# Optimization experiments

Hardware: AMD Instinct MI355X
Metric: run time of the kernel (lower is better)

Reference implementation:

```python
import jax, jax.numpy as jnp
import numpy as np

K, D, H, PD = 512, 512, 512, 128  # nodes, input_dim(=hidden), hidden_dim, pair_dim
P = K * (K - 1)
EPS = 1e-5


def setup_inputs() -> dict:
    key = jax.random.key(0)
    ks = jax.random.split(key, 16)
    s = lambda n: 1.0 / np.sqrt(n)
    return {
        "x": jax.random.normal(ks[0], (K, D), jnp.float32),
        "pair_feats": jax.random.normal(ks[1], (P, PD), jnp.float32),
        "W_att": jax.random.normal(ks[2], (1, 2 * D + PD), jnp.float32) * s(2 * D + PD),
        "b_att": jnp.zeros((1,), jnp.float32),
        "W_obj": jax.random.normal(ks[3], (H, D), jnp.float32) * s(D),
        "b_obj": jnp.zeros((H,), jnp.float32),
        "W_pair": jax.random.normal(ks[4], (H, PD), jnp.float32) * s(PD),
        "b_pair": jnp.zeros((H,), jnp.float32),
        "ln_g": jnp.ones((H,), jnp.float32),
        "ln_b": jnp.zeros((H,), jnp.float32),
        "W1": jax.random.normal(ks[5], (H, H), jnp.float32) * s(H),
        "b1": jnp.zeros((H,), jnp.float32),
        "W2": jax.random.normal(ks[6], (H, H), jnp.float32) * s(H),
        "b2": jnp.zeros((H,), jnp.float32),
    }


def _layernorm(v, g, b):
    mu = jnp.mean(v, axis=-1, keepdims=True)
    var = jnp.mean(jnp.square(v - mu), axis=-1, keepdims=True)
    return g * (v - mu) * jax.lax.rsqrt(var + EPS) + b


def reference(x, pair_feats, W_att, b_att, W_obj, b_obj, W_pair, b_pair,
              ln_g, ln_b, W1, b1, W2, b2):
    k = x.shape[0]
    # j index for each (i, slot t): j = t + (t >= i), i.e. all j != i, ascending
    t = jnp.arange(k - 1)
    j_idx = t[None, :] + (t[None, :] >= jnp.arange(k)[:, None])  # [K, K-1]

    # split the att_mlp weight to avoid materializing cat([x_i, x_j, pair])
    wa, wb, wc = W_att[0, :D], W_att[0, D:2 * D], W_att[0, 2 * D:]
    sa = x @ wa                                           # [K]
    sb = x @ wb                                           # [K]
    pf = pair_feats.reshape(k, k - 1, PD)                 # row-major (i, j!=i)
    sc = jnp.einsum('ktp,p->kt', pf, wc)                  # [K, K-1]
    alpha = jax.nn.sigmoid(sa[:, None] + sb[j_idx] + sc + b_att[0])  # [K, K-1]

    oj = x @ W_obj.T + b_obj                              # [K, H]
    pp = jnp.einsum('ktp,hp->kth', pf, W_pair) + b_pair   # [K, K-1, H]
    messages = jnp.mean(alpha[..., None] * (oj[j_idx] + pp), axis=1)  # [K, H]

    out = _layernorm(x + messages, ln_g, ln_b)
    ffn = jax.nn.relu(out @ W1.T + b1) @ W2.T + b2
    out = _layernorm(out + ffn, ln_g, ln_b)
    return out
```

## Files before the change

### kernel.cpp

```cpp
#include <hip/hip_runtime.h>
#include <math.h>

#define KK 512
#define DD 512
#define HH 512
#define PD 128
#define KM1 511
#define LN_EPS 1e-5f
#define NCHUNK 4
#define CHUNK_T 128

typedef __attribute__((ext_vector_type(8))) short sh8;
typedef __attribute__((ext_vector_type(4))) short sh4;
typedef __attribute__((ext_vector_type(4))) float fx4;

#define MFMA16(a, b, c) __builtin_amdgcn_mfma_f32_16x16x32_bf16(a, b, c, 0, 0, 0)

__device__ __forceinline__ float wave_reduce_sum(float v) {
    #pragma unroll
    for (int off = 32; off > 0; off >>= 1)
        v += __shfl_xor(v, off, 64);
    return v;
}

__device__ __forceinline__ float half_reduce_sum(float v) {
    #pragma unroll
    for (int off = 16; off > 0; off >>= 1)
        v += __shfl_xor(v, off, 64);
    return v;
}

__device__ __forceinline__ short f2bf(float f) {
    unsigned u = __float_as_uint(f);
    u += 0x7fff + ((u >> 16) & 1);
    return (short)(u >> 16);
}

__device__ __forceinline__ sh8 load_cvt8(const float* p) {
    float4 v0 = *(const float4*)p;
    float4 v1 = *(const float4*)(p + 4);
    sh8 r;
    r[0] = f2bf(v0.x); r[1] = f2bf(v0.y); r[2] = f2bf(v0.z); r[3] = f2bf(v0.w);
    r[4] = f2bf(v1.x); r[5] = f2bf(v1.y); r[6] = f2bf(v1.z); r[7] = f2bf(v1.w);
    return r;
}

__global__ __launch_bounds__(256) void prep_w(const float* __restrict__ W_obj,
                                              const float* __restrict__ W_pair,
                                              const float* __restrict__ W1,
                                              const float* __restrict__ W2,
                                              short* __restrict__ W_objb,
                                              short* __restrict__ W_pairb,
                                              short* __restrict__ W1b,
                                              short* __restrict__ W2b) {
    int i = blockIdx.x * 256 + threadIdx.x;
    const float* src; short* dst; int j;
    if (i < 65536)       { src = W_obj;  dst = W_objb;  j = i; }
    else if (i < 81920)  { src = W_pair; dst = W_pairb; j = i - 65536; }
    else if (i < 147456) { src = W1;     dst = W1b;     j = i - 81920; }
    else                 { src = W2;     dst = W2b;     j = i - 147456; }
    float4 v = ((const float4*)src)[j];
    sh4 s;
    s[0] = f2bf(v.x); s[1] = f2bf(v.y); s[2] = f2bf(v.z); s[3] = f2bf(v.w);
    ((sh4*)dst)[j] = s;
}

__global__ __launch_bounds__(64) void sab_kernel(const float* __restrict__ x,
                                                 const float* __restrict__ W_att,
                                                 float* __restrict__ sa,
                                                 float* __restrict__ sb) {
    int k = blockIdx.x;
    int lane = threadIdx.x;
    const float4* xr = (const float4*)(x + (size_t)k * DD);
    const float4* wa = (const float4*)(W_att);
    const float4* wb = (const float4*)(W_att + DD);
    float pa = 0.f, pb = 0.f;
    #pragma unroll
    for (int i = 0; i < 2; i++) {
        float4 xv = xr[lane + i * 64];
        float4 av = wa[lane + i * 64];
        float4 bv = wb[lane + i * 64];
        pa += xv.x * av.x + xv.y * av.y + xv.z * av.z + xv.w * av.w;
        pb += xv.x * bv.x + xv.y * bv.y + xv.z * bv.z + xv.w * bv.w;
    }
    pa = wave_reduce_sum(pa);
    pb = wave_reduce_sum(pb);
    if (lane == 0) { sa[k] = pa; sb[k] = pb; }
}

__global__ __launch_bounds__(512) void pair_pass_kernel(
    const float* __restrict__ pf, const float* __restrict__ sa,
    const float* __restrict__ sb, const float* __restrict__ W_att,
    const float* __restrict__ b_att, float* __restrict__ A,
    float* __restrict__ apf_part, float* __restrict__ asum_part) {
    int k = blockIdx.x;
    int chunk = blockIdx.y;
    int tbase = chunk * CHUNK_T;
    int tid = threadIdx.x;
    int w = tid >> 6, lane = tid & 63;
    int h = lane >> 5, c = lane & 31;
    int g = w * 2 + h;

    float4 wc4 = ((const float4*)(W_att + 2 * DD))[c];
    float sak = sa[k];
    float batt = b_att[0];
    const float4* pfk = (const float4*)(pf + (size_t)k * KM1 * PD);

    float4 v[8];
    int tr[8];
    #pragma unroll
    for (int it = 0; it < 8; it++) {
        int t = tbase + it * 16 + g;
        tr[it] = t;
        int tc = t < KM1 ? t : KM1 - 1;
        v[it] = pfk[(size_t)tc * 32 + c];
    }

    float a0 = 0.f, a1 = 0.f, a2 = 0.f, a3 = 0.f, asl = 0.f;
    #pragma unroll
    for (int it = 0; it < 8; it++) {
        float part = v[it].x * wc4.x + v[it].y * wc4.y + v[it].z * wc4.z + v[it].w * wc4.w;
        part = half_reduce_sum(part);
        int t = tr[it];
        int j = t + (t >= k);
        int jj = j < KK ? j : KK - 1;
        float z = sak + sb[jj] + part + batt;
        float alpha = (t < KM1) ? 1.f / (1.f + __expf(-z)) : 0.f;
        if (c == 0 && t < KM1) A[(size_t)k * KK + j] = alpha;
        a0 += alpha * v[it].x;
        a1 += alpha * v[it].y;
        a2 += alpha * v[it].z;
        a3 += alpha * v[it].w;
        asl += alpha;
    }

    __shared__ float apf_s[16][128];
    __shared__ float asum_s[16];
    apf_s[g][4 * c + 0] = a0;
    apf_s[g][4 * c + 1] = a1;
    apf_s[g][4 * c + 2] = a2;
    apf_s[g][4 * c + 3] = a3;
    if (c == 0) asum_s[g] = asl;
    __syncthreads();
    if (tid < PD) {
        float s = 0.f;
        #pragma unroll
        for (int i = 0; i < 16; i++) s += apf_s[i][tid];
        apf_part[((size_t)chunk * KK + k) * PD + tid] = s;
    }
    if (tid == 0) {
        float s = 0.f;
        #pragma unroll
        for (int i = 0; i < 16; i++) s += asum_s[i];
        asum_part[(size_t)chunk * KK + k] = s;
        if (chunk == 0) A[(size_t)k * KK + k] = 0.f;
    }
}

__global__ __launch_bounds__(128) void k_oj(const float* __restrict__ x,
                                            const short* __restrict__ W_objb,
                                            const float* __restrict__ b_obj,
                                            short* __restrict__ ojT) {
    int m0 = blockIdx.y * 32, n0 = blockIdx.x * 32;
    int tid = threadIdx.x;
    int wv = tid >> 6, l = tid & 63;
    int lr = l & 15, lk = (l >> 4) * 8;
    int mw = m0 + wv * 16;
    fx4 acc[2] = {};
    for (int k0 = 0; k0 < DD; k0 += 32) {
        sh8 a  = load_cvt8(&x[(size_t)(mw + lr) * DD + k0 + lk]);
        sh8 b0 = *(const sh8*)&W_objb[(size_t)(n0 + lr) * DD + k0 + lk];
        sh8 b1 = *(const sh8*)&W_objb[(size_t)(n0 + 16 + lr) * DD + k0 + lk];
        acc[0] = MFMA16(a, b0, acc[0]);
        acc[1] = MFMA16(a, b1, acc[1]);
    }
    __shared__ short tile[32][40];
    int lm4 = (l >> 4) * 4;
    #pragma unroll
    for (int cf = 0; cf < 2; cf++) {
        int col = cf * 16 + lr;
        float bo = b_obj[n0 + col];
        #pragma unroll
        for (int r = 0; r < 4; r++)
            tile[col][wv * 16 + lm4 + r] = f2bf(acc[cf][r] + bo);
    }
    __syncthreads();
    int col = tid >> 2, ro = (tid & 3) * 8;
    *(sh8*)&ojT[(size_t)(n0 + col) * KK + m0 + ro] = *(sh8*)&tile[col][ro];
}

__global__ __launch_bounds__(128) void k_msg(const float* __restrict__ A,
                                             const short* __restrict__ ojT,
                                             const float* __restrict__ apf_part,
                                             const short* __restrict__ W_pairb,
                                             float* __restrict__ msg) {
    int m0 = blockIdx.y * 32, n0 = blockIdx.x * 32;
    int tid = threadIdx.x;
    int wv = tid >> 6, l = tid & 63;
    int lr = l & 15, lk = (l >> 4) * 8;
    int mw = m0 + wv * 16;
    fx4 acc[2] = {};
    for (int k0 = 0; k0 < KK; k0 += 32) {
        sh8 a  = load_cvt8(&A[(size_t)(mw + lr) * KK + k0 + lk]);
        sh8 b0 = *(const sh8*)&ojT[(size_t)(n0 + lr) * KK + k0 + lk];
        sh8 b1 = *(const sh8*)&ojT[(size_t)(n0 + 16 + lr) * KK + k0 + lk];
        acc[0] = MFMA16(a, b0, acc[0]);
        acc[1] = MFMA16(a, b1, acc[1]);
    }
    for (int k0 = 0; k0 < PD; k0 += 32) {
        int p = k0 + lk;
        int row = mw + lr;
        float4 u0 = make_float4(0.f, 0.f, 0.f, 0.f);
        float4 u1 = make_float4(0.f, 0.f, 0.f, 0.f);
        #pragma unroll
        for (int c = 0; c < NCHUNK; c++) {
            const float* pp = &apf_part[((size_t)c * KK + row) * PD + p];
            float4 w0 = *(const float4*)pp;
            float4 w1 = *(const float4*)(pp + 4);
            u0.x += w0.x; u0.y += w0.y; u0.z += w0.z; u0.w += w0.w;
            u1.x += w1.x; u1.y += w1.y; u1.z += w1.z; u1.w += w1.w;
        }
        sh8 a;
        a[0] = f2bf(u0.x); a[1] = f2bf(u0.y); a[2] = f2bf(u0.z); a[3] = f2bf(u0.w);
        a[4] = f2bf(u1.x); a[5] = f2bf(u1.y); a[6] = f2bf(u1.z); a[7] = f2bf(u1.w);
        sh8 b0 = *(const sh8*)&W_pairb[(size_t)(n0 + lr) * PD + p];
        sh8 b1 = *(const sh8*)&W_pairb[(size_t)(n0 + 16 + lr) * PD + p];
        acc[0] = MFMA16(a, b0, acc[0]);
        acc[1] = MFMA16(a, b1, acc[1]);
    }
    __shared__ float tile[32][36];
    int lm4 = (l >> 4) * 4;
    #pragma unroll
    for (int cf = 0; cf < 2; cf++)
        #pragma unroll
        for (int r = 0; r < 4; r++)
            tile[wv * 16 + lm4 + r][cf * 16 + lr] = acc[cf][r];
    __syncthreads();
    for (int q = tid; q < 256; q += 128) {
        int row = q >> 3, c4 = q & 7;
        *(float4*)&msg[(size_t)(m0 + row) * HH + n0 + c4 * 4] = *(float4*)&tile[row][c4 * 4];
    }
}

__global__ __launch_bounds__(128) void ln1_kernel(
    const float* __restrict__ msg, const float* __restrict__ x,
    const float* __restrict__ asum_part, const float* __restrict__ b_pair,
    const float* __restrict__ ln_g, const float* __restrict__ ln_b,
    float* __restrict__ out1, short* __restrict__ out1b) {
    int k = blockIdx.x;
    int tid = threadIdx.x;
    int wv = tid >> 6, l = tid & 63;
    float as = asum_part[k] + asum_part[KK + k] + asum_part[2 * KK + k] + asum_part[3 * KK + k];
    float4 m  = ((const float4*)(msg + (size_t)k * HH))[tid];
    float4 bp = ((const float4*)b_pair)[tid];
    float4 xr = ((const float4*)(x + (size_t)k * DD))[tid];
    const float inv = 1.0f / (float)KM1;
    float4 v;
    v.x = xr.x + (m.x + as * bp.x) * inv;
    v.y = xr.y + (m.y + as * bp.y) * inv;
    v.z = xr.z + (m.z + as * bp.z) * inv;
    v.w = xr.w + (m.w + as * bp.w) * inv;
    float s1 = v.x + v.y + v.z + v.w;
    float s2 = v.x * v.x + v.y * v.y + v.z * v.z + v.w * v.w;
    s1 = wave_reduce_sum(s1);
    s2 = wave_reduce_sum(s2);
    __shared__ float r1[2], r2[2];
    if (l == 0) { r1[wv] = s1; r2[wv] = s2; }
    __syncthreads();
    float S1 = r1[0] + r1[1], S2 = r2[0] + r2[1];
    float mu = S1 * (1.0f / HH);
    float var = S2 * (1.0f / HH) - mu * mu;
    float rs = rsqrtf(var + LN_EPS);
    float4 g4 = ((const float4*)ln_g)[tid];
    float4 b4 = ((const float4*)ln_b)[tid];
    float4 o;
    o.x = g4.x * (v.x - mu) * rs + b4.x;
    o.y = g4.y * (v.y - mu) * rs + b4.y;
    o.z = g4.z * (v.z - mu) * rs + b4.z;
    o.w = g4.w * (v.w - mu) * rs + b4.w;
    ((float4*)(out1 + (size_t)k * HH))[tid] = o;
    sh4 s;
    s[0] = f2bf(o.x); s[1] = f2bf(o.y); s[2] = f2bf(o.z); s[3] = f2bf(o.w);
    ((sh4*)(out1b + (size_t)k * HH))[tid] = s;
}

__global__ __launch_bounds__(128) void k_ffn1(const short* __restrict__ out1b,
                                              const short* __restrict__ W1b,
                                              const float* __restrict__ b1,
                                              short* __restrict__ h1b) {
    int m0 = blockIdx.y * 32, n0 = blockIdx.x * 32;
    int tid = threadIdx.x;
    int wv = tid >> 6, l = tid & 63;
    int lr = l & 15, lk = (l >> 4) * 8;
    int mw = m0 + wv * 16;
    fx4 acc[2] = {};
    for (int k0 = 0; k0 < HH; k0 += 32) {
        sh8 a  = *(const sh8*)&out1b[(size_t)(mw + lr) * HH + k0 + lk];
        sh8 b0 = *(const sh8*)&W1b[(size_t)(n0 + lr) * HH + k0 + lk];
        sh8 b1 = *(const sh8*)&W1b[(size_t)(n0 + 16 + lr) * HH + k0 + lk];
        acc[0] = MFMA16(a, b0, acc[0]);
        acc[1] = MFMA16(a, b1, acc[1]);
    }
    __shared__ short tile[32][40];
    int lm4 = (l >> 4) * 4;
    #pragma unroll
    for (int cf = 0; cf < 2; cf++) {
        int col = cf * 16 + lr;
        float bb = b1[n0 + col];
        #pragma unroll
        for (int r = 0; r < 4; r++)
            tile[wv * 16 + lm4 + r][col] = f2bf(fmaxf(acc[cf][r] + bb, 0.f));
    }
    __syncthreads();
    int row = tid >> 2, co = (tid & 3) * 8;
    *(sh8*)&h1b[(size_t)(m0 + row) * HH + n0 + co] = *(sh8*)&tile[row][co];
}

__global__ __launch_bounds__(128) void k_ffn2(const short* __restrict__ h1b,
                                              const short* __restrict__ W2b,
                                              float* __restrict__ ffn) {
    int m0 = blockIdx.y * 32, n0 = blockIdx.x * 32;
    int tid = threadIdx.x;
    int wv = tid >> 6, l = tid & 63;
    int lr = l & 15, lk = (l >> 4) * 8;
    int mw = m0 + wv * 16;
    fx4 acc[2] = {};
    for (int k0 = 0; k0 < HH; k0 += 32) {
        sh8 a  = *(const sh8*)&h1b[(size_t)(mw + lr) * HH + k0 + lk];
        sh8 b0 = *(const sh8*)&W2b[(size_t)(n0 + lr) * HH + k0 + lk];
        sh8 b1 = *(const sh8*)&W2b[(size_t)(n0 + 16 + lr) * HH + k0 + lk];
        acc[0] = MFMA16(a, b0, acc[0]);
        acc[1] = MFMA16(a, b1, acc[1]);
    }
    __shared__ float tile[32][36];
    int lm4 = (l >> 4) * 4;
    #pragma unroll
    for (int cf = 0; cf < 2; cf++)
        #pragma unroll
        for (int r = 0; r < 4; r++)
            tile[wv * 16 + lm4 + r][cf * 16 + lr] = acc[cf][r];
    __syncthreads();
    for (int q = tid; q < 256; q += 128) {
        int row = q >> 3, c4 = q & 7;
        *(float4*)&ffn[(size_t)(m0 + row) * HH + n0 + c4 * 4] = *(float4*)&tile[row][c4 * 4];
    }
}

__global__ __launch_bounds__(128) void ln2_kernel(
    const float* __restrict__ ffn, const float* __restrict__ out1,
    const float* __restrict__ b2, const float* __restrict__ ln_g,
    const float* __restrict__ ln_b, float* __restrict__ out) {
    int k = blockIdx.x;
    int tid = threadIdx.x;
    int wv = tid >> 6, l = tid & 63;
    float4 f  = ((const float4*)(ffn + (size_t)k * HH))[tid];
    float4 xr = ((const float4*)(out1 + (size_t)k * HH))[tid];
    float4 bb = ((const float4*)b2)[tid];
    float4 v;
    v.x = xr.x + f.x + bb.x;
    v.y = xr.y + f.y + bb.y;
    v.z = xr.z + f.z + bb.z;
    v.w = xr.w + f.w + bb.w;
    float s1 = v.x + v.y + v.z + v.w;
    float s2 = v.x * v.x + v.y * v.y + v.z * v.z + v.w * v.w;
    s1 = wave_reduce_sum(s1);
    s2 = wave_reduce_sum(s2);
    __shared__ float r1[2], r2[2];
    if (l == 0) { r1[wv] = s1; r2[wv] = s2; }
    __syncthreads();
    float S1 = r1[0] + r1[1], S2 = r2[0] + r2[1];
    float mu = S1 * (1.0f / HH);
    float var = S2 * (1.0f / HH) - mu * mu;
    float rs = rsqrtf(var + LN_EPS);
    float4 g4 = ((const float4*)ln_g)[tid];
    float4 b4 = ((const float4*)ln_b)[tid];
    float4 o;
    o.x = g4.x * (v.x - mu) * rs + b4.x;
    o.y = g4.y * (v.y - mu) * rs + b4.y;
    o.z = g4.z * (v.z - mu) * rs + b4.z;
    o.w = g4.w * (v.w - mu) * rs + b4.w;
    ((float4*)(out + (size_t)k * HH))[tid] = o;
}

extern "C" void kernel_launch(void* const* d_in, const int* in_sizes, int n_in,
                              void* d_out, int out_size, void* d_ws, size_t ws_size,
                              hipStream_t stream) {
    const float* x          = (const float*)d_in[0];
    const float* pair_feats = (const float*)d_in[1];
    const float* W_att      = (const float*)d_in[2];
    const float* b_att      = (const float*)d_in[3];
    const float* W_obj      = (const float*)d_in[4];
    const float* b_obj      = (const float*)d_in[5];
    const float* W_pair     = (const float*)d_in[6];
    const float* b_pair     = (const float*)d_in[7];
    const float* ln_g       = (const float*)d_in[8];
    const float* ln_b       = (const float*)d_in[9];
    const float* W1         = (const float*)d_in[10];
    const float* b1         = (const float*)d_in[11];
    const float* W2         = (const float*)d_in[12];
    const float* b2         = (const float*)d_in[13];
    float* out = (float*)d_out;

    const size_t MAT = (size_t)KK * HH;
    float* ws        = (float*)d_ws;
    float* sa        = ws;
    float* sb        = sa + KK;
    float* asum_part = sb + KK;
    float* A         = asum_part + NCHUNK * KK;
    float* apf_part  = A + MAT;
    float* msg       = apf_part + (size_t)NCHUNK * KK * PD;
    float* out1      = msg + MAT;
    float* ffn       = out1 + MAT;
    short* W_objb    = (short*)(ffn + MAT);
    short* W_pairb   = W_objb + MAT;
    short* W1b       = W_pairb + (size_t)HH * PD;
    short* W2b       = W1b + MAT;
    short* ojT       = W2b + MAT;
    short* out1b     = ojT + MAT;
    short* h1b       = out1b + MAT;

    prep_w<<<832, 256, 0, stream>>>(W_obj, W_pair, W1, W2, W_objb, W_pairb, W1b, W2b);
    sab_kernel<<<512, 64, 0, stream>>>(x, W_att, sa, sb);
    pair_pass_kernel<<<dim3(512, NCHUNK), 512, 0, stream>>>(pair_feats, sa, sb, W_att, b_att,
                                                            A, apf_part, asum_part);
    k_oj<<<dim3(16, 16), 128, 0, stream>>>(x, W_objb, b_obj, ojT);
    k_msg<<<dim3(16, 16), 128, 0, stream>>>(A, ojT, apf_part, W_pairb, msg);
    ln1_kernel<<<512, 128, 0, stream>>>(msg, x, asum_part, b_pair, ln_g, ln_b, out1, out1b);
    k_ffn1<<<dim3(16, 16), 128, 0, stream>>>(out1b, W1b, b1, h1b);
    k_ffn2<<<dim3(16, 16), 128, 0, stream>>>(h1b, W2b, ffn);
    ln2_kernel<<<512, 128, 0, stream>>>(ffn, out1, b2, ln_g, ln_b, out);
}
```

Before: 73.61 us.

## Fuse tail GEMM and layernorm kernels into one cooperative kernel with grid syncs

Result: slower. 208.6 us (+183.4%).

```diff
diff --git a/kernel.cpp b/kernel.cpp
--- a/kernel.cpp
+++ b/kernel.cpp
@@ -1,5 +1,8 @@
 #include <hip/hip_runtime.h>
+#include <hip/hip_cooperative_groups.h>
 #include <math.h>
+
+namespace cg = cooperative_groups;
 
 #define KK 512
 #define DD 512
@@ -45,47 +48,44 @@
     return r;
 }
 
-__global__ __launch_bounds__(256) void prep_w(const float* __restrict__ W_obj,
-                                              const float* __restrict__ W_pair,
-                                              const float* __restrict__ W1,
-                                              const float* __restrict__ W2,
-                                              short* __restrict__ W_objb,
-                                              short* __restrict__ W_pairb,
-                                              short* __restrict__ W1b,
-                                              short* __restrict__ W2b) {
-    int i = blockIdx.x * 256 + threadIdx.x;
-    const float* src; short* dst; int j;
-    if (i < 65536)       { src = W_obj;  dst = W_objb;  j = i; }
-    else if (i < 81920)  { src = W_pair; dst = W_pairb; j = i - 65536; }
-    else if (i < 147456) { src = W1;     dst = W1b;     j = i - 81920; }
-    else                 { src = W2;     dst = W2b;     j = i - 147456; }
-    float4 v = ((const float4*)src)[j];
-    sh4 s;
-    s[0] = f2bf(v.x); s[1] = f2bf(v.y); s[2] = f2bf(v.z); s[3] = f2bf(v.w);
-    ((sh4*)dst)[j] = s;
-}
-
-__global__ __launch_bounds__(64) void sab_kernel(const float* __restrict__ x,
-                                                 const float* __restrict__ W_att,
-                                                 float* __restrict__ sa,
-                                                 float* __restrict__ sb) {
-    int k = blockIdx.x;
-    int lane = threadIdx.x;
-    const float4* xr = (const float4*)(x + (size_t)k * DD);
-    const float4* wa = (const float4*)(W_att);
-    const float4* wb = (const float4*)(W_att + DD);
-    float pa = 0.f, pb = 0.f;
-    #pragma unroll
-    for (int i = 0; i < 2; i++) {
-        float4 xv = xr[lane + i * 64];
-        float4 av = wa[lane + i * 64];
-        float4 bv = wb[lane + i * 64];
-        pa += xv.x * av.x + xv.y * av.y + xv.z * av.z + xv.w * av.w;
-        pb += xv.x * bv.x + xv.y * bv.y + xv.z * bv.z + xv.w * bv.w;
-    }
-    pa = wave_reduce_sum(pa);
-    pb = wave_reduce_sum(pb);
-    if (lane == 0) { sa[k] = pa; sb[k] = pb; }
+__global__ __launch_bounds__(256) void prep_sab(
+    const float* __restrict__ W_obj, const float* __restrict__ W_pair,
+    const float* __restrict__ W1, const float* __restrict__ W2,
+    short* __restrict__ W_objb, short* __restrict__ W_pairb,
+    short* __restrict__ W1b, short* __restrict__ W2b,
+    const float* __restrict__ x, const float* __restrict__ W_att,
+    float* __restrict__ sa, float* __restrict__ sb) {
+    int bid = blockIdx.x;
+    if (bid < 832) {
+        int i = bid * 256 + threadIdx.x;
+        const float* src; short* dst; int j;
+        if (i < 65536)       { src = W_obj;  dst = W_objb;  j = i; }
+        else if (i < 81920)  { src = W_pair; dst = W_pairb; j = i - 65536; }
+        else if (i < 147456) { src = W1;     dst = W1b;     j = i - 81920; }
+        else                 { src = W2;     dst = W2b;     j = i - 147456; }
+        float4 v = ((const float4*)src)[j];
+        sh4 s;
+        s[0] = f2bf(v.x); s[1] = f2bf(v.y); s[2] = f2bf(v.z); s[3] = f2bf(v.w);
+        ((sh4*)dst)[j] = s;
+    } else {
+        int w = threadIdx.x >> 6, lane = threadIdx.x & 63;
+        int k = (bid - 832) * 4 + w;
+        const float4* xr = (const float4*)(x + (size_t)k * DD);
+        const float4* wa = (const float4*)(W_att);
+        const float4* wb = (const float4*)(W_att + DD);
+        float pa = 0.f, pb = 0.f;
+        #pragma unroll
+        for (int i = 0; i < 2; i++) {
+            float4 xv = xr[lane + i * 64];
+            float4 av = wa[lane + i * 64];
+            float4 bv = wb[lane + i * 64];
+            pa += xv.x * av.x + xv.y * av.y + xv.z * av.z + xv.w * av.w;
+            pb += xv.x * bv.x + xv.y * bv.y + xv.z * bv.z + xv.w * bv.w;
+        }
+        pa = wave_reduce_sum(pa);
+        pb = wave_reduce_sum(pb);
+        if (lane == 0) { sa[k] = pa; sb[k] = pb; }
+    }
 }
 
 __global__ __launch_bounds__(512) void pair_pass_kernel(
@@ -157,229 +157,232 @@
     }
 }
 
-__global__ __launch_bounds__(128) void k_oj(const float* __restrict__ x,
-                                            const short* __restrict__ W_objb,
-                                            const float* __restrict__ b_obj,
-                                            short* __restrict__ ojT) {
-    int m0 = blockIdx.y * 32, n0 = blockIdx.x * 32;
+__global__ __launch_bounds__(512) void mega_tail(
+    const float* __restrict__ x, const short* __restrict__ W_objb,
+    const float* __restrict__ b_obj, short* __restrict__ ojT,
+    const float* __restrict__ A, const float* __restrict__ apf_part,
+    const short* __restrict__ W_pairb, float* __restrict__ msg,
+    const float* __restrict__ asum_part, const float* __restrict__ b_pair,
+    const float* __restrict__ ln_g, const float* __restrict__ ln_b,
+    float* __restrict__ out1, short* __restrict__ out1b,
+    const short* __restrict__ W1b, const float* __restrict__ b1,
+    short* __restrict__ h1b, const short* __restrict__ W2b,
+    const float* __restrict__ b2, float* __restrict__ ffn,
+    float* __restrict__ out) {
+    cg::grid_group grid = cg::this_grid();
+    int b = blockIdx.x;
     int tid = threadIdx.x;
+    int bx = b & 15, by = b >> 4;
+    int m0 = by * 32, n0 = bx * 32;
     int wv = tid >> 6, l = tid & 63;
     int lr = l & 15, lk = (l >> 4) * 8;
+    int lm4 = (l >> 4) * 4;
     int mw = m0 + wv * 16;
-    fx4 acc[2] = {};
-    for (int k0 = 0; k0 < DD; k0 += 32) {
-        sh8 a  = load_cvt8(&x[(size_t)(mw + lr) * DD + k0 + lk]);
-        sh8 b0 = *(const sh8*)&W_objb[(size_t)(n0 + lr) * DD + k0 + lk];
-        sh8 b1 = *(const sh8*)&W_objb[(size_t)(n0 + 16 + lr) * DD + k0 + lk];
-        acc[0] = MFMA16(a, b0, acc[0]);
-        acc[1] = MFMA16(a, b1, acc[1]);
-    }
-    __shared__ short tile[32][40];
-    int lm4 = (l >> 4) * 4;
-    #pragma unroll
-    for (int cf = 0; cf < 2; cf++) {
-        int col = cf * 16 + lr;
-        float bo = b_obj[n0 + col];
-        #pragma unroll
-        for (int r = 0; r < 4; r++)
-            tile[col][wv * 16 + lm4 + r] = f2bf(acc[cf][r] + bo);
-    }
-    __syncthreads();
-    int col = tid >> 2, ro = (tid & 3) * 8;
-    *(sh8*)&ojT[(size_t)(n0 + col) * KK + m0 + ro] = *(sh8*)&tile[col][ro];
-}
-
-__global__ __launch_bounds__(128) void k_msg(const float* __restrict__ A,
-                                             const short* __restrict__ ojT,
-                                             const float* __restrict__ apf_part,
-                                             const short* __restrict__ W_pairb,
-                                             float* __restrict__ msg) {
-    int m0 = blockIdx.y * 32, n0 = blockIdx.x * 32;
-    int tid = threadIdx.x;
-    int wv = tid >> 6, l = tid & 63;
-    int lr = l & 15, lk = (l >> 4) * 8;
-    int mw = m0 + wv * 16;
-    fx4 acc[2] = {};
-    for (int k0 = 0; k0 < KK; k0 += 32) {
-        sh8 a  = load_cvt8(&A[(size_t)(mw + lr) * KK + k0 + lk]);
-        sh8 b0 = *(const sh8*)&ojT[(size_t)(n0 + lr) * KK + k0 + lk];
-        sh8 b1 = *(const sh8*)&ojT[(size_t)(n0 + 16 + lr) * KK + k0 + lk];
-        acc[0] = MFMA16(a, b0, acc[0]);
-        acc[1] = MFMA16(a, b1, acc[1]);
-    }
-    for (int k0 = 0; k0 < PD; k0 += 32) {
-        int p = k0 + lk;
-        int row = mw + lr;
-        float4 u0 = make_float4(0.f, 0.f, 0.f, 0.f);
-        float4 u1 = make_float4(0.f, 0.f, 0.f, 0.f);
-        #pragma unroll
-        for (int c = 0; c < NCHUNK; c++) {
-            const float* pp = &apf_part[((size_t)c * KK + row) * PD + p];
-            float4 w0 = *(const float4*)pp;
-            float4 w1 = *(const float4*)(pp + 4);
-            u0.x += w0.x; u0.y += w0.y; u0.z += w0.z; u0.w += w0.w;
-            u1.x += w1.x; u1.y += w1.y; u1.z += w1.z; u1.w += w1.w;
-        }
-        sh8 a;
-        a[0] = f2bf(u0.x); a[1] = f2bf(u0.y); a[2] = f2bf(u0.z); a[3] = f2bf(u0.w);
-        a[4] = f2bf(u1.x); a[5] = f2bf(u1.y); a[6] = f2bf(u1.z); a[7] = f2bf(u1.w);
-        sh8 b0 = *(const sh8*)&W_pairb[(size_t)(n0 + lr) * PD + p];
-        sh8 b1 = *(const sh8*)&W_pairb[(size_t)(n0 + 16 + lr) * PD + p];
-        acc[0] = MFMA16(a, b0, acc[0]);
-        acc[1] = MFMA16(a, b1, acc[1]);
-    }
-    __shared__ float tile[32][36];
-    int lm4 = (l >> 4) * 4;
-    #pragma unroll
-    for (int cf = 0; cf < 2; cf++)
-        #pragma unroll
-        for (int r = 0; r < 4; r++)
-            tile[wv * 16 + lm4 + r][cf * 16 + lr] = acc[cf][r];
-    __syncthreads();
-    for (int q = tid; q < 256; q += 128) {
-        int row = q >> 3, c4 = q & 7;
-        *(float4*)&msg[(size_t)(m0 + row) * HH + n0 + c4 * 4] = *(float4*)&tile[row][c4 * 4];
-    }
-}
-
-__global__ __launch_bounds__(128) void ln1_kernel(
-    const float* __restrict__ msg, const float* __restrict__ x,
-    const float* __restrict__ asum_part, const float* __restrict__ b_pair,
-    const float* __restrict__ ln_g, const float* __restrict__ ln_b,
-    float* __restrict__ out1, short* __restrict__ out1b) {
-    int k = blockIdx.x;
-    int tid = threadIdx.x;
-    int wv = tid >> 6, l = tid & 63;
-    float as = asum_part[k] + asum_part[KK + k] + asum_part[2 * KK + k] + asum_part[3 * KK + k];
-    float4 m  = ((const float4*)(msg + (size_t)k * HH))[tid];
-    float4 bp = ((const float4*)b_pair)[tid];
-    float4 xr = ((const float4*)(x + (size_t)k * DD))[tid];
-    const float inv = 1.0f / (float)KM1;
-    float4 v;
-    v.x = xr.x + (m.x + as * bp.x) * inv;
-    v.y = xr.y + (m.y + as * bp.y) * inv;
-    v.z = xr.z + (m.z + as * bp.z) * inv;
-    v.w = xr.w + (m.w + as * bp.w) * inv;
-    float s1 = v.x + v.y + v.z + v.w;
-    float s2 = v.x * v.x + v.y * v.y + v.z * v.z + v.w * v.w;
-    s1 = wave_reduce_sum(s1);
-    s2 = wave_reduce_sum(s2);
-    __shared__ float r1[2], r2[2];
-    if (l == 0) { r1[wv] = s1; r2[wv] = s2; }
-    __syncthreads();
-    float S1 = r1[0] + r1[1], S2 = r2[0] + r2[1];
-    float mu = S1 * (1.0f / HH);
-    float var = S2 * (1.0f / HH) - mu * mu;
-    float rs = rsqrtf(var + LN_EPS);
-    float4 g4 = ((const float4*)ln_g)[tid];
-    float4 b4 = ((const float4*)ln_b)[tid];
-    float4 o;
-    o.x = g4.x * (v.x - mu) * rs + b4.x;
-    o.y = g4.y * (v.y - mu) * rs + b4.y;
-    o.z = g4.z * (v.z - mu) * rs + b4.z;
-    o.w = g4.w * (v.w - mu) * rs + b4.w;
-    ((float4*)(out1 + (size_t)k * HH))[tid] = o;
-    sh4 s;
-    s[0] = f2bf(o.x); s[1] = f2bf(o.y); s[2] = f2bf(o.z); s[3] = f2bf(o.w);
-    ((sh4*)(out1b + (size_t)k * HH))[tid] = s;
-}
-
-__global__ __launch_bounds__(128) void k_ffn1(const short* __restrict__ out1b,
-                                              const short* __restrict__ W1b,
-                                              const float* __restrict__ b1,
-                                              short* __restrict__ h1b) {
-    int m0 = blockIdx.y * 32, n0 = blockIdx.x * 32;
-    int tid = threadIdx.x;
-    int wv = tid >> 6, l = tid & 63;
-    int lr = l & 15, lk = (l >> 4) * 8;
-    int mw = m0 + wv * 16;
-    fx4 acc[2] = {};
-    for (int k0 = 0; k0 < HH; k0 += 32) {
-        sh8 a  = *(const sh8*)&out1b[(size_t)(mw + lr) * HH + k0 + lk];
-        sh8 b0 = *(const sh8*)&W1b[(size_t)(n0 + lr) * HH + k0 + lk];
-        sh8 b1 = *(const sh8*)&W1b[(size_t)(n0 + 16 + lr) * HH + k0 + lk];
-        acc[0] = MFMA16(a, b0, acc[0]);
-        acc[1] = MFMA16(a, b1, acc[1]);
-    }
-    __shared__ short tile[32][40];
-    int lm4 = (l >> 4) * 4;
-    #pragma unroll
-    for (int cf = 0; cf < 2; cf++) {
-        int col = cf * 16 + lr;
-        float bb = b1[n0 + col];
-        #pragma unroll
-        for (int r = 0; r < 4; r++)
-            tile[wv * 16 + lm4 + r][col] = f2bf(fmaxf(acc[cf][r] + bb, 0.f));
-    }
-    __syncthreads();
-    int row = tid >> 2, co = (tid & 3) * 8;
-    *(sh8*)&h1b[(size_t)(m0 + row) * HH + n0 + co] = *(sh8*)&tile[row][co];
-}
-
-__global__ __launch_bounds__(128) void k_ffn2(const short* __restrict__ h1b,
-                                              const short* __restrict__ W2b,
-                                              float* __restrict__ ffn) {
-    int m0 = blockIdx.y * 32, n0 = blockIdx.x * 32;
-    int tid = threadIdx.x;
-    int wv = tid >> 6, l = tid & 63;
-    int lr = l & 15, lk = (l >> 4) * 8;
-    int mw = m0 + wv * 16;
-    fx4 acc[2] = {};
-    for (int k0 = 0; k0 < HH; k0 += 32) {
-        sh8 a  = *(const sh8*)&h1b[(size_t)(mw + lr) * HH + k0 + lk];
-        sh8 b0 = *(const sh8*)&W2b[(size_t)(n0 + lr) * HH + k0 + lk];
-        sh8 b1 = *(const sh8*)&W2b[(size_t)(n0 + 16 + lr) * HH + k0 + lk];
-        acc[0] = MFMA16(a, b0, acc[0]);
-        acc[1] = MFMA16(a, b1, acc[1]);
-    }
-    __shared__ float tile[32][36];
-    int lm4 = (l >> 4) * 4;
-    #pragma unroll
-    for (int cf = 0; cf < 2; cf++)
-        #pragma unroll
-        for (int r = 0; r < 4; r++)
-            tile[wv * 16 + lm4 + r][cf * 16 + lr] = acc[cf][r];
-    __syncthreads();
-    for (int q = tid; q < 256; q += 128) {
-        int row = q >> 3, c4 = q & 7;
-        *(float4*)&ffn[(size_t)(m0 + row) * HH + n0 + c4 * 4] = *(float4*)&tile[row][c4 * 4];
-    }
-}
-
-__global__ __launch_bounds__(128) void ln2_kernel(
-    const float* __restrict__ ffn, const float* __restrict__ out1,
-    const float* __restrict__ b2, const float* __restrict__ ln_g,
-    const float* __restrict__ ln_b, float* __restrict__ out) {
-    int k = blockIdx.x;
-    int tid = threadIdx.x;
-    int wv = tid >> 6, l = tid & 63;
-    float4 f  = ((const float4*)(ffn + (size_t)k * HH))[tid];
-    float4 xr = ((const float4*)(out1 + (size_t)k * HH))[tid];
-    float4 bb = ((const float4*)b2)[tid];
-    float4 v;
-    v.x = xr.x + f.x + bb.x;
-    v.y = xr.y + f.y + bb.y;
-    v.z = xr.z + f.z + bb.z;
-    v.w = xr.w + f.w + bb.w;
-    float s1 = v.x + v.y + v.z + v.w;
-    float s2 = v.x * v.x + v.y * v.y + v.z * v.z + v.w * v.w;
-    s1 = wave_reduce_sum(s1);
-    s2 = wave_reduce_sum(s2);
-    __shared__ float r1[2], r2[2];
-    if (l == 0) { r1[wv] = s1; r2[wv] = s2; }
-    __syncthreads();
-    float S1 = r1[0] + r1[1], S2 = r2[0] + r2[1];
-    float mu = S1 * (1.0f / HH);
-    float var = S2 * (1.0f / HH) - mu * mu;
-    float rs = rsqrtf(var + LN_EPS);
-    float4 g4 = ((const float4*)ln_g)[tid];
-    float4 b4 = ((const float4*)ln_b)[tid];
-    float4 o;
-    o.x = g4.x * (v.x - mu) * rs + b4.x;
-    o.y = g4.y * (v.y - mu) * rs + b4.y;
-    o.z = g4.z * (v.z - mu) * rs + b4.z;
-    o.w = g4.w * (v.w - mu) * rs + b4.w;
-    ((float4*)(out + (size_t)k * HH))[tid] = o;
+
+    __shared__ short tileS[32][40];
+    __shared__ float tileF[32][36];
+    __shared__ float r1s[2][2], r2s[2][2];
+
+    if (tid < 128) {
+        fx4 acc[2] = {};
+        for (int k0 = 0; k0 < DD; k0 += 32) {
+            sh8 a   = load_cvt8(&x[(size_t)(mw + lr) * DD + k0 + lk]);
+            sh8 b0  = *(const sh8*)&W_objb[(size_t)(n0 + lr) * DD + k0 + lk];
+            sh8 b1v = *(const sh8*)&W_objb[(size_t)(n0 + 16 + lr) * DD + k0 + lk];
+            acc[0] = MFMA16(a, b0, acc[0]);
+            acc[1] = MFMA16(a, b1v, acc[1]);
+        }
+        #pragma unroll
+        for (int cf = 0; cf < 2; cf++) {
+            int col = cf * 16 + lr;
+            float bo = b_obj[n0 + col];
+            #pragma unroll
+            for (int r = 0; r < 4; r++)
+                tileS[col][wv * 16 + lm4 + r] = f2bf(acc[cf][r] + bo);
+        }
+    }
+    __syncthreads();
+    if (tid < 128) {
+        int col = tid >> 2, ro = (tid & 3) * 8;
+        *(sh8*)&ojT[(size_t)(n0 + col) * KK + m0 + ro] = *(sh8*)&tileS[col][ro];
+    }
+    grid.sync();
+
+    if (tid < 128) {
+        fx4 acc[2] = {};
+        for (int k0 = 0; k0 < KK; k0 += 32) {
+            sh8 a   = load_cvt8(&A[(size_t)(mw + lr) * KK + k0 + lk]);
+            sh8 b0  = *(const sh8*)&ojT[(size_t)(n0 + lr) * KK + k0 + lk];
+            sh8 b1v = *(const sh8*)&ojT[(size_t)(n0 + 16 + lr) * KK + k0 + lk];
+            acc[0] = MFMA16(a, b0, acc[0]);
+            acc[1] = MFMA16(a, b1v, acc[1]);
+        }
+        for (int k0 = 0; k0 < PD; k0 += 32) {
+            int p = k0 + lk;
+            int row = mw + lr;
+            float4 u0 = make_float4(0.f, 0.f, 0.f, 0.f);
+            float4 u1 = make_float4(0.f, 0.f, 0.f, 0.f);
+            #pragma unroll
+            for (int cc = 0; cc < NCHUNK; cc++) {
+                const float* pp = &apf_part[((size_t)cc * KK + row) * PD + p];
+                float4 w0 = *(const float4*)pp;
+                float4 w1 = *(const float4*)(pp + 4);
+                u0.x += w0.x; u0.y += w0.y; u0.z += w0.z; u0.w += w0.w;
+                u1.x += w1.x; u1.y += w1.y; u1.z += w1.z; u1.w += w1.w;
+            }
+            sh8 a;
+            a[0] = f2bf(u0.x); a[1] = f2bf(u0.y); a[2] = f2bf(u0.z); a[3] = f2bf(u0.w);
+            a[4] = f2bf(u1.x); a[5] = f2bf(u1.y); a[6] = f2bf(u1.z); a[7] = f2bf(u1.w);
+            sh8 b0  = *(const sh8*)&W_pairb[(size_t)(n0 + lr) * PD + p];
+            sh8 b1v = *(const sh8*)&W_pairb[(size_t)(n0 + 16 + lr) * PD + p];
+            acc[0] = MFMA16(a, b0, acc[0]);
+            acc[1] = MFMA16(a, b1v, acc[1]);
+        }
+        #pragma unroll
+        for (int cf = 0; cf < 2; cf++)
+            #pragma unroll
+            for (int r = 0; r < 4; r++)
+                tileF[wv * 16 + lm4 + r][cf * 16 + lr] = acc[cf][r];
+    }
+    __syncthreads();
+    if (tid < 128) {
+        for (int q = tid; q < 256; q += 128) {
+            int row = q >> 3, c4 = q & 7;
+            *(float4*)&msg[(size_t)(m0 + row) * HH + n0 + c4 * 4] = *(float4*)&tileF[row][c4 * 4];
+        }
+    }
+    grid.sync();
+
+    float4 vC, g4C, b4C;
+    int rgC = 0, kC = 0, t4C = 0;
+    if (tid < 256) {
+        rgC = tid >> 7;
+        kC = 2 * b + rgC;
+        t4C = tid & 127;
+        int wv2 = (tid >> 6) & 1;
+        float as = asum_part[kC] + asum_part[KK + kC] + asum_part[2 * KK + kC] + asum_part[3 * KK + kC];
+        float4 m  = ((const float4*)(msg + (size_t)kC * HH))[t4C];
+        float4 bp = ((const float4*)b_pair)[t4C];
+        float4 xr = ((const float4*)(x + (size_t)kC * DD))[t4C];
+        const float inv = 1.0f / (float)KM1;
+        vC.x = xr.x + (m.x + as * bp.x) * inv;
+        vC.y = xr.y + (m.y + as * bp.y) * inv;
+        vC.z = xr.z + (m.z + as * bp.z) * inv;
+        vC.w = xr.w + (m.w + as * bp.w) * inv;
+        float s1 = vC.x + vC.y + vC.z + vC.w;
+        float s2 = vC.x * vC.x + vC.y * vC.y + vC.z * vC.z + vC.w * vC.w;
+        s1 = wave_reduce_sum(s1);
+        s2 = wave_reduce_sum(s2);
+        if (l == 0) { r1s[rgC][wv2] = s1; r2s[rgC][wv2] = s2; }
+    }
+    __syncthreads();
+    if (tid < 256) {
+        float S1 = r1s[rgC][0] + r1s[rgC][1];
+        float S2 = r2s[rgC][0] + r2s[rgC][1];
+        float mu = S1 * (1.0f / HH);
+        float var = S2 * (1.0f / HH) - mu * mu;
+        float rs = rsqrtf(var + LN_EPS);
+        g4C = ((const float4*)ln_g)[t4C];
+        b4C = ((const float4*)ln_b)[t4C];
+        float4 o;
+        o.x = g4C.x * (vC.x - mu) * rs + b4C.x;
+        o.y = g4C.y * (vC.y - mu) * rs + b4C.y;
+        o.z = g4C.z * (vC.z - mu) * rs + b4C.z;
+        o.w = g4C.w * (vC.w - mu) * rs + b4C.w;
+        ((float4*)(out1 + (size_t)kC * HH))[t4C] = o;
+        sh4 s;
+        s[0] = f2bf(o.x); s[1] = f2bf(o.y); s[2] = f2bf(o.z); s[3] = f2bf(o.w);
+        ((sh4*)(out1b + (size_t)kC * HH))[t4C] = s;
+    }
+    grid.sync();
+
+    if (tid < 128) {
+        fx4 acc[2] = {};
+        for (int k0 = 0; k0 < HH; k0 += 32) {
+            sh8 a   = *(const sh8*)&out1b[(size_t)(mw + lr) * HH + k0 + lk];
+            sh8 b0  = *(const sh8*)&W1b[(size_t)(n0 + lr) * HH + k0 + lk];
+            sh8 b1v = *(const sh8*)&W1b[(size_t)(n0 + 16 + lr) * HH + k0 + lk];
+            acc[0] = MFMA16(a, b0, acc[0]);
+            acc[1] = MFMA16(a, b1v, acc[1]);
+        }
+        #pragma unroll
+        for (int cf = 0; cf < 2; cf++) {
+            int col = cf * 16 + lr;
+            float bb = b1[n0 + col];
+            #pragma unroll
+            for (int r = 0; r < 4; r++)
+                tileS[wv * 16 + lm4 + r][col] = f2bf(fmaxf(acc[cf][r] + bb, 0.f));
+        }
+    }
+    __syncthreads();
+    if (tid < 128) {
+        int row = tid >> 2, co = (tid & 3) * 8;
+        *(sh8*)&h1b[(size_t)(m0 + row) * HH + n0 + co] = *(sh8*)&tileS[row][co];
+    }
+    grid.sync();
+
+    if (tid < 128) {
+        fx4 acc[2] = {};
+        for (int k0 = 0; k0 < HH; k0 += 32) {
+            sh8 a   = *(const sh8*)&h1b[(size_t)(mw + lr) * HH + k0 + lk];
+            sh8 b0  = *(const sh8*)&W2b[(size_t)(n0 + lr) * HH + k0 + lk];
+            sh8 b1v = *(const sh8*)&W2b[(size_t)(n0 + 16 + lr) * HH + k0 + lk];
+            acc[0] = MFMA16(a, b0, acc[0]);
+            acc[1] = MFMA16(a, b1v, acc[1]);
+        }
+        #pragma unroll
+        for (int cf = 0; cf < 2; cf++)
+            #pragma unroll
+            for (int r = 0; r < 4; r++)
+                tileF[wv * 16 + lm4 + r][cf * 16 + lr] = acc[cf][r];
+    }
+    __syncthreads();
+    if (tid < 128) {
+        for (int q = tid; q < 256; q += 128) {
+            int row = q >> 3, c4 = q & 7;
+            *(float4*)&ffn[(size_t)(m0 + row) * HH + n0 + c4 * 4] = *(float4*)&tileF[row][c4 * 4];
+        }
+    }
+    grid.sync();
+
+    float4 vF;
+    if (tid < 256) {
+        int rg = tid >> 7;
+        int k = 2 * b + rg;
+        int t4 = tid & 127;
+        int wv2 = (tid >> 6) & 1;
+        float4 f  = ((const float4*)(ffn + (size_t)k * HH))[t4];
+        float4 xr = ((const float4*)(out1 + (size_t)k * HH))[t4];
+        float4 bb = ((const float4*)b2)[t4];
+        vF.x = xr.x + f.x + bb.x;
+        vF.y = xr.y + f.y + bb.y;
+        vF.z = xr.z + f.z + bb.z;
+        vF.w = xr.w + f.w + bb.w;
+        float s1 = vF.x + vF.y + vF.z + vF.w;
+        float s2 = vF.x * vF.x + vF.y * vF.y + vF.z * vF.z + vF.w * vF.w;
+        s1 = wave_reduce_sum(s1);
+        s2 = wave_reduce_sum(s2);
+        if (l == 0) { r1s[rg][wv2] = s1; r2s[rg][wv2] = s2; }
+    }
+    __syncthreads();
+    if (tid < 256) {
+        int rg = tid >> 7;
+        int k = 2 * b + rg;
+        int t4 = tid & 127;
+        float S1 = r1s[rg][0] + r1s[rg][1];
+        float S2 = r2s[rg][0] + r2s[rg][1];
+        float mu = S1 * (1.0f / HH);
+        float var = S2 * (1.0f / HH) - mu * mu;
+        float rs = rsqrtf(var + LN_EPS);
+        float4 g4 = ((const float4*)ln_g)[t4];
+        float4 b4 = ((const float4*)ln_b)[t4];
+        float4 o;
+        o.x = g4.x * (vF.x - mu) * rs + b4.x;
+        o.y = g4.y * (vF.y - mu) * rs + b4.y;
+        o.z = g4.z * (vF.z - mu) * rs + b4.z;
+        o.w = g4.w * (vF.w - mu) * rs + b4.w;
+        ((float4*)(out + (size_t)k * HH))[t4] = o;
+    }
 }
 
 extern "C" void kernel_launch(void* const* d_in, const int* in_sizes, int n_in,
@@ -419,14 +422,16 @@
     short* out1b     = ojT + MAT;
     short* h1b       = out1b + MAT;
 
-    prep_w<<<832, 256, 0, stream>>>(W_obj, W_pair, W1, W2, W_objb, W_pairb, W1b, W2b);
-    sab_kernel<<<512, 64, 0, stream>>>(x, W_att, sa, sb);
+    prep_sab<<<960, 256, 0, stream>>>(W_obj, W_pair, W1, W2, W_objb, W_pairb, W1b, W2b,
+                                      x, W_att, sa, sb);
     pair_pass_kernel<<<dim3(512, NCHUNK), 512, 0, stream>>>(pair_feats, sa, sb, W_att, b_att,
                                                             A, apf_part, asum_part);
-    k_oj<<<dim3(16, 16), 128, 0, stream>>>(x, W_objb, b_obj, ojT);
-    k_msg<<<dim3(16, 16), 128, 0, stream>>>(A, ojT, apf_part, W_pairb, msg);
-    ln1_kernel<<<512, 128, 0, stream>>>(msg, x, asum_part, b_pair, ln_g, ln_b, out1, out1b);
-    k_ffn1<<<dim3(16, 16), 128, 0, stream>>>(out1b, W1b, b1, h1b);
-    k_ffn2<<<dim3(16, 16), 128, 0, stream>>>(h1b, W2b, ffn);
-    ln2_kernel<<<512, 128, 0, stream>>>(ffn, out1, b2, ln_g, ln_b, out);
-}
+    void* margs[] = {
+        (void*)&x, (void*)&W_objb, (void*)&b_obj, (void*)&ojT,
+        (void*)&A, (void*)&apf_part, (void*)&W_pairb, (void*)&msg,
+        (void*)&asum_part, (void*)&b_pair, (void*)&ln_g, (void*)&ln_b,
+        (void*)&out1, (void*)&out1b, (void*)&W1b, (void*)&b1,
+        (void*)&h1b, (void*)&W2b, (void*)&b2, (void*)&ffn, (void*)&out
+    };
+    hipLaunchCooperativeKernel((void*)mega_tail, dim3(256), dim3(512), margs, 0, stream);
+}
```
